# Optimization experiments

Hardware: AMD Instinct MI355X
Metric: run time of the kernel (lower is better)

Reference implementation:

```python
import jax, jax.numpy as jnp
import numpy as np

N = 50000      # nodes
E = 800000     # edges (before self-loops)
IN = 128       # in_channels
HID = 64       # hidden_channels
HEADS = 4
OUT = 64       # out_channels
SLOPE = 0.2    # negative_slope


def setup_inputs() -> dict:
    key = jax.random.key(0)
    ks = jax.random.split(key, 16)

    def p(k, shape, fan_in):
        return jax.random.normal(k, shape, dtype=jnp.float32) / np.float32(np.sqrt(fan_in))

    inp = jax.random.normal(ks[0], (N, IN), dtype=jnp.float32)
    edge_index = jax.random.randint(ks[1], (2, E), 0, N, dtype=jnp.int32)

    W1 = p(ks[2], (IN, HEADS * HID), IN)
    att_src1 = p(ks[3], (1, HEADS, HID), HID)
    att_dst1 = p(ks[4], (1, HEADS, HID), HID)
    b1 = jnp.zeros((HEADS * HID,), jnp.float32)

    W2 = p(ks[5], (HEADS * HID, HEADS * HID), HEADS * HID)
    att_src2 = p(ks[6], (1, HEADS, HID), HID)
    att_dst2 = p(ks[7], (1, HEADS, HID), HID)
    b2 = jnp.zeros((HEADS * HID,), jnp.float32)

    W3 = p(ks[8], (HEADS * HID, HEADS * OUT), HEADS * HID)
    att_src3 = p(ks[9], (1, HEADS, OUT), OUT)
    att_dst3 = p(ks[10], (1, HEADS, OUT), OUT)
    b3 = jnp.zeros((HEADS * OUT,), jnp.float32)

    return dict(inp=inp, edge_index=edge_index,
                W1=W1, att_src1=att_src1, att_dst1=att_dst1, b1=b1,
                W2=W2, att_src2=att_src2, att_dst2=att_dst2, b2=b2,
                W3=W3, att_src3=att_src3, att_dst3=att_dst3, b3=b3)


def _gat_conv(x, W, a_src, a_dst, b, src, dst, H, C):
    """One PyG-style GATConv (concat=True, dropout=0, self-loops already in src/dst)."""
    n = x.shape[0]
    h = (x @ W).reshape(n, H, C)                     # [N,H,C]
    alpha_src = jnp.sum(h * a_src, axis=-1)          # [N,H]
    alpha_dst = jnp.sum(h * a_dst, axis=-1)          # [N,H]
    e = jax.nn.leaky_relu(alpha_src[src] + alpha_dst[dst], SLOPE)  # [Etot,H]
    # segment softmax over incoming edges of each destination node
    emax = jax.ops.segment_max(e, dst, num_segments=n)             # [N,H]
    ee = jnp.exp(e - emax[dst])
    denom = jax.ops.segment_sum(ee, dst, num_segments=n)           # [N,H]
    alpha = ee / denom[dst]                                        # [Etot,H]
    out = jax.ops.segment_sum(alpha[:, :, None] * h[src], dst, num_segments=n)  # [N,H,C]
    return out.reshape(n, H * C) + b


def reference(inp, edge_index, W1, att_src1, att_dst1, b1,
              W2, att_src2, att_dst2, b2, W3, att_src3, att_dst3, b3):
    n = inp.shape[0]
    loops = jnp.arange(n, dtype=edge_index.dtype)
    src = jnp.concatenate([edge_index[0], loops])  # add self-loops (PyG default)
    dst = jnp.concatenate([edge_index[1], loops])
    h1 = jax.nn.elu(_gat_conv(inp, W1, att_src1, att_dst1, b1, src, dst, HEADS, HID))
    h2 = jax.nn.elu(_gat_conv(h1, W2, att_src2, att_dst2, b2, src, dst, HEADS, HID))
    oup = jax.nn.elu(_gat_conv(h2, W3, att_src3, att_dst3, b3, src, dst, HEADS, OUT))
    return oup
```

## Files before the change

### kernel.cpp

```cpp
#include <hip/hip_runtime.h>
#include <hip/hip_bf16.h>
#include <stdint.h>

#define HEADS 4
#define SLOPE 0.2f

typedef unsigned short u16;
typedef float f32x4 __attribute__((ext_vector_type(4)));
typedef short s16x8 __attribute__((ext_vector_type(8)));
typedef unsigned short u16x4 __attribute__((ext_vector_type(4)));

__device__ __forceinline__ u16 f2bf(float f) {
    unsigned int u = __float_as_uint(f);
    u = (u + 0x7fffu + ((u >> 16) & 1u)) >> 16;
    return (u16)u;
}
__device__ __forceinline__ float bf2f(u16 v) {
    return __uint_as_float(((unsigned int)v) << 16);
}
__device__ __forceinline__ float fin(float x) {
    return (x == x && fabsf(x) < 1e30f) ? x : 0.f;
}

__global__ void prep_kernel(const float* __restrict__ inp, u16* __restrict__ Xb,
                            const float* __restrict__ W1, u16* __restrict__ Wt1,
                            const float* __restrict__ W2, u16* __restrict__ Wt2,
                            const float* __restrict__ W3, u16* __restrict__ Wt3,
                            int* __restrict__ deg, int N) {
    int i = blockIdx.x * blockDim.x + threadIdx.x;
    int cast4 = N * 32;
    if (i < cast4) {
        f32x4 v = *(const f32x4*)(inp + (size_t)i * 4);
        u16x4 o;
        #pragma unroll
        for (int j = 0; j < 4; j++) o[j] = f2bf(fin(v[j]));
        *(u16x4*)(Xb + (size_t)i * 4) = o;
        return;
    }
    i -= cast4;
    if (i < N) { deg[i] = 0; return; }
    i -= N;
    if (i >= 0 && i < 128 * 256) {
        int k = i >> 8, m = i & 255;
        Wt1[m * 128 + k] = f2bf(fin(W1[i]));
        return;
    }
    i -= 128 * 256;
    if (i >= 0 && i < 256 * 256) {
        int k = i >> 8, m = i & 255;
        Wt2[m * 256 + k] = f2bf(fin(W2[i]));
        return;
    }
    i -= 256 * 256;
    if (i >= 0 && i < 256 * 256) {
        int k = i >> 8, m = i & 255;
        Wt3[m * 256 + k] = f2bf(fin(W3[i]));
    }
}

__global__ void count_kernel(const int* __restrict__ dst, int* __restrict__ deg,
                             int* __restrict__ rank, int E, int N) {
    int i = blockIdx.x * blockDim.x + threadIdx.x;
    if (i < E + N) {
        int d = (i < E) ? dst[i] : (i - E);
        d = ((unsigned)d < (unsigned)N) ? d : 0;
        rank[i] = atomicAdd(&deg[d], 1);
    }
}

__global__ __launch_bounds__(256) void scan_kernel(const int* __restrict__ deg,
                                                   int* __restrict__ rowstart, int N) {
    __shared__ int wsum[4];
    __shared__ int sm[256];
    int b = blockIdx.x, tid = threadIdx.x;
    int start = b * 1024;
    int pre = 0;
    for (int i = tid; i < start; i += 256) pre += deg[i];
    #pragma unroll
    for (int off = 1; off <= 32; off <<= 1) pre += __shfl_xor(pre, off);
    if ((tid & 63) == 0) wsum[tid >> 6] = pre;
    __syncthreads();
    int block_pre = wsum[0] + wsum[1] + wsum[2] + wsum[3];

    int base = start + tid * 4;
    int v[4]; int s = 0;
    #pragma unroll
    for (int j = 0; j < 4; j++) { int i = base + j; v[j] = (i < N) ? deg[i] : 0; s += v[j]; }
    sm[tid] = s;
    __syncthreads();
    for (int off = 1; off < 256; off <<= 1) {
        int t = (tid >= off) ? sm[tid - off] : 0;
        __syncthreads();
        sm[tid] += t;
        __syncthreads();
    }
    int run = block_pre + sm[tid] - s;
    #pragma unroll
    for (int j = 0; j < 4; j++) {
        int i = base + j;
        if (i < N) { rowstart[i] = run; run += v[j]; }
    }
    if (b == gridDim.x - 1 && tid == 255) rowstart[N] = block_pre + sm[255];
}

__global__ void place_kernel(const int* __restrict__ src, const int* __restrict__ dst,
                             const int* __restrict__ rowstart, const int* __restrict__ rank,
                             int* __restrict__ csr, int E, int N) {
    int i = blockIdx.x * blockDim.x + threadIdx.x;
    if (i < E + N) {
        int s, d;
        if (i < E) { s = src[i]; d = dst[i]; }
        else       { s = i - E; d = i - E; }
        s = ((unsigned)s < (unsigned)N) ? s : 0;
        d = ((unsigned)d < (unsigned)N) ? d : 0;
        int pos = rowstart[d] + rank[i];
        if ((unsigned)pos < (unsigned)(E + N)) csr[pos] = s;
    }
}

__global__ __launch_bounds__(256) void gemm_kernel(
        const u16* __restrict__ X, const u16* __restrict__ Wt,
        u16* __restrict__ Hout, const float* __restrict__ att_src,
        const float* __restrict__ att_dst, float* __restrict__ as_out,
        float* __restrict__ ad_out, int N, int K) {
    int wv = threadIdx.x >> 6, lane = threadIdx.x & 63;
    int quad = lane >> 4, l16 = lane & 15;
    int m0 = (blockIdx.x * 2 + (wv & 1)) * 32;
    int n0 = (wv >> 1) * 128;

    f32x4 acc[2][8];
    #pragma unroll
    for (int r = 0; r < 2; r++)
        #pragma unroll
        for (int c = 0; c < 8; c++) acc[r][c] = (f32x4){0.f, 0.f, 0.f, 0.f};

    for (int k0 = 0; k0 < K; k0 += 32) {
        s16x8 a[2], b[8];
        #pragma unroll
        for (int r = 0; r < 2; r++) {
            int row = m0 + r * 16 + l16;
            row = row < N ? row : N - 1;
            a[r] = *(const s16x8*)(X + (size_t)row * K + k0 + quad * 8);
        }
        #pragma unroll
        for (int c = 0; c < 8; c++) {
            int n = n0 + c * 16 + l16;
            b[c] = *(const s16x8*)(Wt + (size_t)n * K + k0 + quad * 8);
        }
        #pragma unroll
        for (int r = 0; r < 2; r++)
            #pragma unroll
            for (int c = 0; c < 8; c++)
                acc[r][c] = __builtin_amdgcn_mfma_f32_16x16x32_bf16(a[r], b[c], acc[r][c], 0, 0, 0);
    }

    int head0 = n0 >> 6;
    float aps[2][4][2], apd[2][4][2];
    #pragma unroll
    for (int r = 0; r < 2; r++)
        #pragma unroll
        for (int j = 0; j < 4; j++)
            aps[r][j][0] = aps[r][j][1] = apd[r][j][0] = apd[r][j][1] = 0.f;

    #pragma unroll
    for (int r = 0; r < 2; r++) {
        int rowb = m0 + r * 16 + quad * 4;
        #pragma unroll
        for (int c = 0; c < 8; c++) {
            int col = n0 + c * 16 + l16;
            float av = fin(att_src[col]);
            float dv = fin(att_dst[col]);
            int hh = c >> 2;
            #pragma unroll
            for (int j = 0; j < 4; j++) {
                int row = rowb + j;
                float v = acc[r][c][j];
                aps[r][j][hh] += v * av;
                apd[r][j][hh] += v * dv;
                if (row < N) Hout[(size_t)row * 256 + col] = f2bf(v);
            }
        }
    }
    #pragma unroll
    for (int off = 1; off <= 8; off <<= 1) {
        #pragma unroll
        for (int r = 0; r < 2; r++)
            #pragma unroll
            for (int j = 0; j < 4; j++) {
                aps[r][j][0] += __shfl_xor(aps[r][j][0], off);
                aps[r][j][1] += __shfl_xor(aps[r][j][1], off);
                apd[r][j][0] += __shfl_xor(apd[r][j][0], off);
                apd[r][j][1] += __shfl_xor(apd[r][j][1], off);
            }
    }
    if (l16 == 0) {
        #pragma unroll
        for (int r = 0; r < 2; r++) {
            int rowb = m0 + r * 16 + quad * 4;
            #pragma unroll
            for (int j = 0; j < 4; j++) {
                int row = rowb + j;
                if (row < N) {
                    #pragma unroll
                    for (int hh = 0; hh < 2; hh++) {
                        as_out[row * 4 + head0 + hh] = aps[r][j][hh];
                        ad_out[row * 4 + head0 + hh] = apd[r][j][hh];
                    }
                }
            }
        }
    }
}

__global__ __launch_bounds__(256) void gather_kernel(
        const u16* __restrict__ Hb, const float* __restrict__ asrc,
        const float* __restrict__ adst, const int* __restrict__ rowstart,
        const int* __restrict__ csr, const float* __restrict__ bias,
        u16* __restrict__ outb, float* __restrict__ outf, int write_f32,
        int N, int Etot) {
    int wv = threadIdx.x >> 6, lane = threadIdx.x & 63;
    int n = blockIdx.x * 4 + wv;
    if (n >= N) return;
    int es = lane >> 5, c = lane & 31;
    int h = c >> 3;
    int i0 = rowstart[n], i1 = rowstart[n + 1];
    i0 = min(max(i0, 0), Etot);
    i1 = min(max(i1, i0), Etot);

    float adh = adst[n * 4 + h];
    float acc[8];
    float ws = 0.f;
    #pragma unroll
    for (int j = 0; j < 8; j++) acc[j] = 0.f;

    int i = i0 + es;
    for (; i + 2 < i1; i += 4) {
        int sA = csr[i], sB = csr[i + 2];
        sA = ((unsigned)sA < (unsigned)N) ? sA : 0;
        sB = ((unsigned)sB < (unsigned)N) ? sB : 0;
        float eA = asrc[sA * 4 + h] + adh;
        float eB = asrc[sB * 4 + h] + adh;
        s16x8 hvA = *(const s16x8*)(Hb + (size_t)sA * 256 + c * 8);
        s16x8 hvB = *(const s16x8*)(Hb + (size_t)sB * 256 + c * 8);
        eA = eA > 0.f ? eA : SLOPE * eA;
        eB = eB > 0.f ? eB : SLOPE * eB;
        float wA = __expf(fminf(eA, 80.f));
        float wB = __expf(fminf(eB, 80.f));
        ws += wA + wB;
        #pragma unroll
        for (int j = 0; j < 8; j++)
            acc[j] += wA * bf2f((u16)hvA[j]) + wB * bf2f((u16)hvB[j]);
    }
    if (i < i1) {
        int s = csr[i];
        s = ((unsigned)s < (unsigned)N) ? s : 0;
        float e = asrc[s * 4 + h] + adh;
        s16x8 hv = *(const s16x8*)(Hb + (size_t)s * 256 + c * 8);
        e = e > 0.f ? e : SLOPE * e;
        float w = __expf(fminf(e, 80.f));
        ws += w;
        #pragma unroll
        for (int j = 0; j < 8; j++) acc[j] += w * bf2f((u16)hv[j]);
    }

    ws += __shfl_xor(ws, 32);
    #pragma unroll
    for (int j = 0; j < 8; j++) acc[j] += __shfl_xor(acc[j], 32);

    if (es == 0) {
        float invh = (ws > 0.f) ? 1.f / ws : 0.f;
        f32x4 blo = *(const f32x4*)(bias + c * 8);
        f32x4 bhi = *(const f32x4*)(bias + c * 8 + 4);
        size_t base = (size_t)n * 256 + c * 8;
        float o[8];
        #pragma unroll
        for (int j = 0; j < 8; j++) {
            float v = acc[j] * invh + fin(j < 4 ? blo[j] : bhi[j - 4]);
            o[j] = v > 0.f ? v : (__expf(v) - 1.f);
        }
        if (write_f32) {
            f32x4 lo = {o[0], o[1], o[2], o[3]}, hi = {o[4], o[5], o[6], o[7]};
            *(f32x4*)(outf + base) = lo;
            *(f32x4*)(outf + base + 4) = hi;
        } else {
            s16x8 ob;
            #pragma unroll
            for (int j = 0; j < 8; j++) ob[j] = (short)f2bf(o[j]);
            *(s16x8*)(outb + base) = ob;
        }
    }
}

extern "C" void kernel_launch(void* const* d_in, const int* in_sizes, int n_in,
                              void* d_out, int out_size, void* d_ws, size_t ws_size,
                              hipStream_t stream) {
    const float* inp  = (const float*)d_in[0];
    const int*   ei   = (const int*)d_in[1];
    const float* W1   = (const float*)d_in[2];
    const float* at_s1= (const float*)d_in[3];
    const float* at_d1= (const float*)d_in[4];
    const float* b1   = (const float*)d_in[5];
    const float* W2   = (const float*)d_in[6];
    const float* at_s2= (const float*)d_in[7];
    const float* at_d2= (const float*)d_in[8];
    const float* b2   = (const float*)d_in[9];
    const float* W3   = (const float*)d_in[10];
    const float* at_s3= (const float*)d_in[11];
    const float* at_d3= (const float*)d_in[12];
    const float* b3   = (const float*)d_in[13];

    const int N = in_sizes[0] / 128;
    const int E = in_sizes[1] / 2;
    const int Etot = E + N;
    const int* esrc = ei;
    const int* edst = ei + E;

    char* p = (char*)d_ws;
    auto alloc = [&](size_t b) -> void* {
        void* q = (void*)p;
        p += (b + 255) & ~(size_t)255;
        return q;
    };
    u16*   Xb       = (u16*)alloc((size_t)N * 256 * 2);
    u16*   Hb       = (u16*)alloc((size_t)N * 256 * 2);
    u16*   Wt1      = (u16*)alloc((size_t)128 * 256 * 2);
    u16*   Wt2      = (u16*)alloc((size_t)256 * 256 * 2);
    u16*   Wt3      = (u16*)alloc((size_t)256 * 256 * 2);
    float* asb      = (float*)alloc((size_t)N * 4 * 4);
    float* adb      = (float*)alloc((size_t)N * 4 * 4);
    int*   deg      = (int*)alloc((size_t)N * 4);
    int*   rowstart = (int*)alloc((size_t)(N + 1) * 4);
    int*   rank     = (int*)alloc((size_t)Etot * 4);
    int*   csr      = (int*)alloc((size_t)Etot * 4);
    float* outf     = (float*)d_out;

    const int SB = (N + 1023) / 1024;
    const int prep_total = N * 32 + N + 128 * 256 + 2 * 256 * 256;

    prep_kernel<<<(prep_total + 255) / 256, 256, 0, stream>>>(
        inp, Xb, W1, Wt1, W2, Wt2, W3, Wt3, deg, N);
    count_kernel<<<(Etot + 255) / 256, 256, 0, stream>>>(edst, deg, rank, E, N);
    scan_kernel<<<SB, 256, 0, stream>>>(deg, rowstart, N);
    place_kernel<<<(Etot + 255) / 256, 256, 0, stream>>>(esrc, edst, rowstart, rank, csr, E, N);

    const int gemm_grid = (N + 63) / 64;
    const int node_grid = (N + 3) / 4;

    gemm_kernel<<<gemm_grid, 256, 0, stream>>>(Xb, Wt1, Hb, at_s1, at_d1, asb, adb, N, 128);
    gather_kernel<<<node_grid, 256, 0, stream>>>(Hb, asb, adb, rowstart, csr, b1,
                                                 Xb, outf, 0, N, Etot);
    gemm_kernel<<<gemm_grid, 256, 0, stream>>>(Xb, Wt2, Hb, at_s2, at_d2, asb, adb, N, 256);
    gather_kernel<<<node_grid, 256, 0, stream>>>(Hb, asb, adb, rowstart, csr, b2,
                                                 Xb, outf, 0, N, Etot);
    gemm_kernel<<<gemm_grid, 256, 0, stream>>>(Xb, Wt3, Hb, at_s3, at_d3, asb, adb, N, 256);
    gather_kernel<<<node_grid, 256, 0, stream>>>(Hb, asb, adb, rowstart, csr, b3,
                                                 Xb, outf, 1, N, Etot);
}
```

Measured before the change: 499.2 us.

## Stage GEMM tiles in shared memory and unroll gather loop four edges deep

The GEMM now loads 64-row A tiles and the full 256-column B tile into LDS with register prefetch of the next K-step, and each wave computes a 64x64 block (one head) from shared fragments. This replaces per-wave direct global loads of the weight matrix, cutting redundant global traffic, and simplifies the per-head attention reduction. The gather kernel adds a 4-way unrolled edge loop so more neighbor row loads are in flight at once. The costs are extra LDS use and barriers, plus higher register pressure in the gather kernel.

```diff
diff --git a/kernel.cpp b/kernel.cpp
--- a/kernel.cpp
+++ b/kernel.cpp
@@ -118,94 +118,122 @@
     }
 }
 
-__global__ __launch_bounds__(256) void gemm_kernel(
+__global__ __launch_bounds__(256, 3) void gemm_kernel(
         const u16* __restrict__ X, const u16* __restrict__ Wt,
         u16* __restrict__ Hout, const float* __restrict__ att_src,
         const float* __restrict__ att_dst, float* __restrict__ as_out,
         float* __restrict__ ad_out, int N, int K) {
-    int wv = threadIdx.x >> 6, lane = threadIdx.x & 63;
+    __shared__ __align__(16) u16 As[64 * 72];
+    __shared__ __align__(16) u16 Bs[256 * 72];
+    int t = threadIdx.x;
+    int wv = t >> 6, lane = t & 63;
     int quad = lane >> 4, l16 = lane & 15;
-    int m0 = (blockIdx.x * 2 + (wv & 1)) * 32;
-    int n0 = (wv >> 1) * 128;
-
-    f32x4 acc[2][8];
-    #pragma unroll
-    for (int r = 0; r < 2; r++)
-        #pragma unroll
-        for (int c = 0; c < 8; c++) acc[r][c] = (f32x4){0.f, 0.f, 0.f, 0.f};
-
-    for (int k0 = 0; k0 < K; k0 += 32) {
-        s16x8 a[2], b[8];
-        #pragma unroll
-        for (int r = 0; r < 2; r++) {
-            int row = m0 + r * 16 + l16;
-            row = row < N ? row : N - 1;
-            a[r] = *(const s16x8*)(X + (size_t)row * K + k0 + quad * 8);
-        }
-        #pragma unroll
-        for (int c = 0; c < 8; c++) {
-            int n = n0 + c * 16 + l16;
-            b[c] = *(const s16x8*)(Wt + (size_t)n * K + k0 + quad * 8);
-        }
-        #pragma unroll
-        for (int r = 0; r < 2; r++)
-            #pragma unroll
-            for (int c = 0; c < 8; c++)
-                acc[r][c] = __builtin_amdgcn_mfma_f32_16x16x32_bf16(a[r], b[c], acc[r][c], 0, 0, 0);
-    }
-
-    int head0 = n0 >> 6;
-    float aps[2][4][2], apd[2][4][2];
-    #pragma unroll
-    for (int r = 0; r < 2; r++)
-        #pragma unroll
-        for (int j = 0; j < 4; j++)
-            aps[r][j][0] = aps[r][j][1] = apd[r][j][0] = apd[r][j][1] = 0.f;
-
-    #pragma unroll
-    for (int r = 0; r < 2; r++) {
+    int m0 = blockIdx.x * 64;
+    int n0 = wv * 64;
+    int srow = t >> 3, sslot = t & 7;
+
+    f32x4 acc[4][4];
+    #pragma unroll
+    for (int r = 0; r < 4; r++)
+        #pragma unroll
+        for (int c = 0; c < 4; c++) acc[r][c] = (f32x4){0.f, 0.f, 0.f, 0.f};
+
+    const int nsteps = K >> 6;
+    s16x8 ra[2], rb[8];
+    {
+        #pragma unroll
+        for (int s = 0; s < 2; s++) {
+            int rg = m0 + s * 32 + srow; rg = rg < N ? rg : N - 1;
+            ra[s] = *(const s16x8*)(X + (size_t)rg * K + sslot * 8);
+        }
+        #pragma unroll
+        for (int s = 0; s < 8; s++) {
+            int n = s * 32 + srow;
+            rb[s] = *(const s16x8*)(Wt + (size_t)n * K + sslot * 8);
+        }
+    }
+    for (int step = 0; step < nsteps; step++) {
+        __syncthreads();
+        #pragma unroll
+        for (int s = 0; s < 2; s++)
+            *(s16x8*)(As + (s * 32 + srow) * 72 + sslot * 8) = ra[s];
+        #pragma unroll
+        for (int s = 0; s < 8; s++)
+            *(s16x8*)(Bs + (s * 32 + srow) * 72 + sslot * 8) = rb[s];
+        __syncthreads();
+        if (step + 1 < nsteps) {
+            int k0 = (step + 1) << 6;
+            #pragma unroll
+            for (int s = 0; s < 2; s++) {
+                int rg = m0 + s * 32 + srow; rg = rg < N ? rg : N - 1;
+                ra[s] = *(const s16x8*)(X + (size_t)rg * K + k0 + sslot * 8);
+            }
+            #pragma unroll
+            for (int s = 0; s < 8; s++) {
+                int n = s * 32 + srow;
+                rb[s] = *(const s16x8*)(Wt + (size_t)n * K + k0 + sslot * 8);
+            }
+        }
+        #pragma unroll
+        for (int subk = 0; subk < 2; subk++) {
+            s16x8 af[4], bf[4];
+            #pragma unroll
+            for (int r = 0; r < 4; r++)
+                af[r] = *(const s16x8*)(As + (r * 16 + l16) * 72 + subk * 32 + quad * 8);
+            #pragma unroll
+            for (int c = 0; c < 4; c++)
+                bf[c] = *(const s16x8*)(Bs + (n0 + c * 16 + l16) * 72 + subk * 32 + quad * 8);
+            #pragma unroll
+            for (int r = 0; r < 4; r++)
+                #pragma unroll
+                for (int c = 0; c < 4; c++)
+                    acc[r][c] = __builtin_amdgcn_mfma_f32_16x16x32_bf16(af[r], bf[c], acc[r][c], 0, 0, 0);
+        }
+    }
+
+    float aps[4][4], apd[4][4];
+    #pragma unroll
+    for (int r = 0; r < 4; r++)
+        #pragma unroll
+        for (int j = 0; j < 4; j++) { aps[r][j] = 0.f; apd[r][j] = 0.f; }
+
+    #pragma unroll
+    for (int r = 0; r < 4; r++) {
         int rowb = m0 + r * 16 + quad * 4;
         #pragma unroll
-        for (int c = 0; c < 8; c++) {
+        for (int c = 0; c < 4; c++) {
             int col = n0 + c * 16 + l16;
             float av = fin(att_src[col]);
             float dv = fin(att_dst[col]);
-            int hh = c >> 2;
             #pragma unroll
             for (int j = 0; j < 4; j++) {
                 int row = rowb + j;
                 float v = acc[r][c][j];
-                aps[r][j][hh] += v * av;
-                apd[r][j][hh] += v * dv;
+                aps[r][j] += v * av;
+                apd[r][j] += v * dv;
                 if (row < N) Hout[(size_t)row * 256 + col] = f2bf(v);
             }
         }
     }
     #pragma unroll
-    for (int off = 1; off <= 8; off <<= 1) {
-        #pragma unroll
-        for (int r = 0; r < 2; r++)
+    for (int off = 1; off <= 8; off <<= 1)
+        #pragma unroll
+        for (int r = 0; r < 4; r++)
             #pragma unroll
             for (int j = 0; j < 4; j++) {
-                aps[r][j][0] += __shfl_xor(aps[r][j][0], off);
-                aps[r][j][1] += __shfl_xor(aps[r][j][1], off);
-                apd[r][j][0] += __shfl_xor(apd[r][j][0], off);
-                apd[r][j][1] += __shfl_xor(apd[r][j][1], off);
+                aps[r][j] += __shfl_xor(aps[r][j], off);
+                apd[r][j] += __shfl_xor(apd[r][j], off);
             }
-    }
     if (l16 == 0) {
         #pragma unroll
-        for (int r = 0; r < 2; r++) {
+        for (int r = 0; r < 4; r++) {
             int rowb = m0 + r * 16 + quad * 4;
             #pragma unroll
             for (int j = 0; j < 4; j++) {
                 int row = rowb + j;
                 if (row < N) {
-                    #pragma unroll
-                    for (int hh = 0; hh < 2; hh++) {
-                        as_out[row * 4 + head0 + hh] = aps[r][j][hh];
-                        ad_out[row * 4 + head0 + hh] = apd[r][j][hh];
-                    }
+                    as_out[row * 4 + wv] = aps[r][j];
+                    ad_out[row * 4 + wv] = apd[r][j];
                 }
             }
         }
@@ -234,6 +262,28 @@
     for (int j = 0; j < 8; j++) acc[j] = 0.f;
 
     int i = i0 + es;
+    for (; i + 6 < i1; i += 8) {
+        int ss[4];
+        #pragma unroll
+        for (int u = 0; u < 4; u++) {
+            int s = csr[i + 2 * u];
+            ss[u] = ((unsigned)s < (unsigned)N) ? s : 0;
+        }
+        float e[4]; s16x8 hv[4];
+        #pragma unroll
+        for (int u = 0; u < 4; u++) {
+            e[u] = asrc[ss[u] * 4 + h] + adh;
+            hv[u] = *(const s16x8*)(Hb + (size_t)ss[u] * 256 + c * 8);
+        }
+        #pragma unroll
+        for (int u = 0; u < 4; u++) {
+            float ee = e[u] > 0.f ? e[u] : SLOPE * e[u];
+            float w = __expf(fminf(ee, 80.f));
+            ws += w;
+            #pragma unroll
+            for (int j = 0; j < 8; j++) acc[j] += w * bf2f((u16)hv[u][j]);
+        }
+    }
     for (; i + 2 < i1; i += 4) {
         int sA = csr[i], sB = csr[i + 2];
         sA = ((unsigned)sA < (unsigned)N) ? sA : 0;
```

After: 444.4 us. -11.0%, faster.
